# Optimization experiments

Measured on AMD Instinct MI355X. Metric: run time of the kernel, lower is better.

The kernel has to match this reference:

```python
import jax, jax.numpy as jnp
import numpy as np

N_T, N_I = 4096, 4096
TEXT_DIM, IMAGE_DIM, HIDDEN_DIM = 1024, 1024, 1024


def setup_inputs() -> dict:
    key = jax.random.key(0)
    ks = jax.random.split(key, 8)
    s_t = 1.0 / np.sqrt(TEXT_DIM)
    s_i = 1.0 / np.sqrt(IMAGE_DIM)
    return {
        "text_features": jax.random.normal(ks[0], (N_T, TEXT_DIM), jnp.float32),
        "image_features": jax.random.normal(ks[1], (N_I, IMAGE_DIM), jnp.float32),
        # nn.Linear params: weight [out, in], bias [out]
        "w_text": jax.random.uniform(ks[2], (HIDDEN_DIM, TEXT_DIM), jnp.float32, -s_t, s_t),
        "b_text": jax.random.uniform(ks[3], (HIDDEN_DIM,), jnp.float32, -s_t, s_t),
        "w_image": jax.random.uniform(ks[4], (HIDDEN_DIM, IMAGE_DIM), jnp.float32, -s_i, s_i),
        "b_image": jax.random.uniform(ks[5], (HIDDEN_DIM,), jnp.float32, -s_i, s_i),
        "scale_TI": jnp.ones((1,), jnp.float32),
        "scale_IT": jnp.ones((1,), jnp.float32),
    }


def reference(text_features, image_features, w_text, b_text, w_image, b_image, scale_TI, scale_IT):
    # linear projections to shared hidden space
    t = text_features @ w_text.T + b_text      # [N_t, H]
    i = image_features @ w_image.T + b_image   # [N_i, H]
    inv_sqrt_h = 1.0 / jnp.sqrt(jnp.asarray(HIDDEN_DIM, t.dtype))
    # text -> image attention: softmax over image axis, scaled post-softmax
    logits_TI = (t @ i.T) * inv_sqrt_h               # [N_t, N_i]
    attn_TI = jax.nn.softmax(logits_TI, axis=-1) * scale_TI
    # image -> text attention
    attn_IT = jax.nn.softmax(logits_TI.T, axis=-1) * scale_IT  # [N_i, N_t]
    text_attention_on_image = attn_TI @ image_features  # [N_t, image_dim]
    image_attention_on_text = attn_IT @ text_features   # [N_i, text_dim]
    return (text_attention_on_image, image_attention_on_text)
```

## Files before the change

### kernel.cpp

```cpp
#include <hip/hip_runtime.h>


typedef __bf16 bf16x8 __attribute__((ext_vector_type(8)));
typedef float f32x4 __attribute__((ext_vector_type(4)));

#define N_T 4096
#define N_I 4096
#define DIM 1024
#define TSS 136

__device__ __forceinline__ unsigned short f2bf(float f) {
    unsigned int u = __float_as_uint(f);
    u += 0x7fffu + ((u >> 16) & 1u);
    return (unsigned short)(u >> 16);
}

__device__ __forceinline__ void async_cp16(const unsigned short* g, unsigned short* l) {
    __builtin_amdgcn_global_load_lds(
        (const __attribute__((address_space(1))) unsigned int*)g,
        (__attribute__((address_space(3))) unsigned int*)l, 16, 0, 0);
}

__device__ __forceinline__ void stage_async(const unsigned short* __restrict__ src,
                                            int ld, int row0, int k0,
                                            unsigned short* lds, int tid) {
    int r = tid >> 2, c = (tid & 3) << 3;
    const unsigned short* g = src + (size_t)(row0 + r) * ld + k0 + c;
    async_cp16(g, lds + r * 32 + c);
    async_cp16(g + (size_t)64 * ld, lds + (64 + r) * 32 + c);
}

__device__ __forceinline__ void mfma_step(const unsigned short* As,
                                          const unsigned short* Bs, f32x4 acc[4][4],
                                          int wrow, int wcol, int lane16, int quad) {
    bf16x8 a[4], b[4];
#pragma unroll
    for (int i = 0; i < 4; ++i) {
        a[i] = *(const bf16x8*)&As[(wrow + i * 16 + lane16) * 32 + quad * 8];
        b[i] = *(const bf16x8*)&Bs[(wcol + i * 16 + lane16) * 32 + quad * 8];
    }
#pragma unroll
    for (int i = 0; i < 4; ++i)
#pragma unroll
        for (int j = 0; j < 4; ++j)
            acc[i][j] = __builtin_amdgcn_mfma_f32_16x16x32_bf16(a[i], b[j], acc[i][j], 0, 0, 0);
}

__device__ __forceinline__ void tile_store(const unsigned short* sm,
                                           unsigned short* __restrict__ g, int ld,
                                           int row0, int col0, int tid) {
    int r = tid >> 1, h = (tid & 1) << 6;
    const unsigned short* src = sm + r * TSS + h;
    unsigned short* dst = g + (size_t)(row0 + r) * ld + col0 + h;
#pragma unroll
    for (int v = 0; v < 8; ++v)
        *(uint4*)(dst + v * 8) = *(const uint4*)(src + v * 8);
}

#define GEMM_IDX()                                               \
    int tid = threadIdx.x;                                       \
    int m0 = blockIdx.x * 128, n0 = blockIdx.y * 128;            \
    int lane = tid & 63, wave = tid >> 6;                        \
    int lane16 = lane & 15, quad = lane >> 4;                    \
    int wrow = (wave >> 1) * 64, wcol = (wave & 1) * 64;         \
    f32x4 acc[4][4];                                             \
    {                                                            \
        f32x4 z = {0.f, 0.f, 0.f, 0.f};                          \
        for (int i = 0; i < 4; ++i)                              \
            for (int j = 0; j < 4; ++j) acc[i][j] = z;           \
    }

__global__ void __launch_bounds__(256)
cvt_bf16_all(const float* __restrict__ t, const float* __restrict__ im,
             const float* __restrict__ wt, const float* __restrict__ wi,
             unsigned short* __restrict__ tb, unsigned short* __restrict__ imb,
             unsigned short* __restrict__ wtb, unsigned short* __restrict__ wib) {
    size_t i = (size_t)(blockIdx.x * 256 + threadIdx.x) * 8;
    const float* s;
    unsigned short* d;
    size_t off;
    if (i < 4194304)       { s = t;  d = tb;  off = i; }
    else if (i < 8388608)  { s = im; d = imb; off = i - 4194304; }
    else if (i < 9437184)  { s = wt; d = wtb; off = i - 8388608; }
    else                   { s = wi; d = wib; off = i - 9437184; }
    float4 f0 = *(const float4*)(s + off);
    float4 f1 = *(const float4*)(s + off + 4);
    uint4 o;
    o.x = (unsigned int)f2bf(f0.x) | ((unsigned int)f2bf(f0.y) << 16);
    o.y = (unsigned int)f2bf(f0.z) | ((unsigned int)f2bf(f0.w) << 16);
    o.z = (unsigned int)f2bf(f1.x) | ((unsigned int)f2bf(f1.y) << 16);
    o.w = (unsigned int)f2bf(f1.z) | ((unsigned int)f2bf(f1.w) << 16);
    *(uint4*)(d + off) = o;
}

__global__ void __launch_bounds__(256)
transpose_cvt2(const float* __restrict__ im, const float* __restrict__ tx,
               unsigned short* __restrict__ imgT, unsigned short* __restrict__ textT) {
    const float* in = blockIdx.z ? tx : im;
    unsigned short* out = blockIdx.z ? textT : imgT;
    __shared__ float tile[32][33];
    int c0 = blockIdx.x * 32, r0 = blockIdx.y * 32;
    int txi = threadIdx.x & 31, tyi = threadIdx.x >> 5;
#pragma unroll
    for (int i = tyi; i < 32; i += 8)
        tile[i][txi] = in[(size_t)(r0 + i) * DIM + c0 + txi];
    __syncthreads();
#pragma unroll
    for (int i = tyi; i < 32; i += 8)
        out[(size_t)(c0 + i) * N_T + r0 + txi] = f2bf(tile[txi][i]);
}

__global__ void __launch_bounds__(256, 2)
gemm_proj2(const unsigned short* __restrict__ Atx, const unsigned short* __restrict__ Wtx,
           const float* __restrict__ btx, unsigned short* __restrict__ Ctx,
           const unsigned short* __restrict__ Aim, const unsigned short* __restrict__ Wim,
           const float* __restrict__ bim, unsigned short* __restrict__ Cim) {
    __shared__ unsigned short As[128 * 32];
    __shared__ unsigned short Bs[128 * 32];
    int z = blockIdx.z;
    const unsigned short* A = z ? Aim : Atx;
    const unsigned short* W = z ? Wim : Wtx;
    const float* bias = z ? bim : btx;
    unsigned short* C = z ? Cim : Ctx;
    GEMM_IDX();
    for (int k0 = 0; k0 < DIM; k0 += 32) {
        stage_async(A, DIM, m0, k0, As, tid);
        stage_async(W, DIM, n0, k0, Bs, tid);
        __syncthreads();
        mfma_step(As, Bs, acc, wrow, wcol, lane16, quad);
        __syncthreads();
    }
#pragma unroll
    for (int j = 0; j < 4; ++j) {
        int col = n0 + wcol + j * 16 + lane16;
        float bv = bias[col];
#pragma unroll
        for (int i = 0; i < 4; ++i) {
            int rowb = m0 + wrow + i * 16 + quad * 4;
#pragma unroll
            for (int r = 0; r < 4; ++r)
                C[(size_t)(rowb + r) * DIM + col] = f2bf(acc[i][j][r] + bv);
        }
    }
}

__global__ void __launch_bounds__(256, 2)
gemm_logits_exp(const unsigned short* __restrict__ Tb,
                const unsigned short* __restrict__ Ib,
                unsigned short* __restrict__ P, unsigned short* __restrict__ PT,
                float* __restrict__ lT, float* __restrict__ lI) {
    __shared__ unsigned short smem[128 * TSS];
    unsigned short* As = smem;
    unsigned short* Bs = smem + 128 * 32;
    GEMM_IDX();
    for (int k0 = 0; k0 < DIM; k0 += 32) {
        stage_async(Tb, DIM, m0, k0, As, tid);
        stage_async(Ib, DIM, n0, k0, Bs, tid);
        __syncthreads();
        mfma_step(As, Bs, acc, wrow, wcol, lane16, quad);
        __syncthreads();
    }
#pragma unroll
    for (int i = 0; i < 4; ++i)
#pragma unroll
        for (int j = 0; j < 4; ++j)
#pragma unroll
            for (int r = 0; r < 4; ++r)
                acc[i][j][r] = __expf(acc[i][j][r] * 0.03125f);
#pragma unroll
    for (int i = 0; i < 4; ++i)
#pragma unroll
        for (int r = 0; r < 4; ++r) {
            float s = acc[i][0][r] + acc[i][1][r] + acc[i][2][r] + acc[i][3][r];
            s += __shfl_xor(s, 1); s += __shfl_xor(s, 2);
            s += __shfl_xor(s, 4); s += __shfl_xor(s, 8);
            if (lane16 == 0) atomicAdd(&lT[m0 + wrow + i * 16 + quad * 4 + r], s);
        }
#pragma unroll
    for (int j = 0; j < 4; ++j) {
        float s = 0.f;
#pragma unroll
        for (int i = 0; i < 4; ++i)
#pragma unroll
            for (int r = 0; r < 4; ++r) s += acc[i][j][r];
        s += __shfl_xor(s, 16); s += __shfl_xor(s, 32);
        if (quad == 0) atomicAdd(&lI[n0 + wcol + j * 16 + lane16], s);
    }
    __syncthreads();
#pragma unroll
    for (int i = 0; i < 4; ++i)
#pragma unroll
        for (int j = 0; j < 4; ++j)
#pragma unroll
            for (int r = 0; r < 4; ++r)
                smem[(wrow + i * 16 + quad * 4 + r) * TSS + wcol + j * 16 + lane16] =
                    f2bf(acc[i][j][r]);
    __syncthreads();
    tile_store(smem, P, N_I, m0, n0, tid);
    __syncthreads();
#pragma unroll
    for (int i = 0; i < 4; ++i)
#pragma unroll
        for (int j = 0; j < 4; ++j) {
            unsigned int lo = (unsigned int)f2bf(acc[i][j][0]) |
                              ((unsigned int)f2bf(acc[i][j][1]) << 16);
            unsigned int hi = (unsigned int)f2bf(acc[i][j][2]) |
                              ((unsigned int)f2bf(acc[i][j][3]) << 16);
            uint2 v; v.x = lo; v.y = hi;
            *(uint2*)&smem[(wcol + j * 16 + lane16) * TSS + wrow + i * 16 + quad * 4] = v;
        }
    __syncthreads();
    tile_store(smem, PT, N_T, n0, m0, tid);
}

__global__ void __launch_bounds__(256, 2)
gemm_attn2(const unsigned short* __restrict__ P, const unsigned short* __restrict__ imgT,
           const float* __restrict__ lT, const float* __restrict__ sTI,
           float* __restrict__ out0,
           const unsigned short* __restrict__ PT, const unsigned short* __restrict__ textT,
           const float* __restrict__ lI, const float* __restrict__ sIT,
           float* __restrict__ out1) {
    __shared__ unsigned short As[128 * 32];
    __shared__ unsigned short Bs[128 * 32];
    int which = blockIdx.z;
    const unsigned short* A = which ? PT : P;
    const unsigned short* Bt = which ? textT : imgT;
    const float* l = which ? lI : lT;
    const float* sp = which ? sIT : sTI;
    float* out = which ? out1 : out0;
    GEMM_IDX();
    for (int k0 = 0; k0 < 4096; k0 += 32) {
        stage_async(A, 4096, m0, k0, As, tid);
        stage_async(Bt, 4096, n0, k0, Bs, tid);
        __syncthreads();
        mfma_step(As, Bs, acc, wrow, wcol, lane16, quad);
        __syncthreads();
    }
    float sc = sp[0];
#pragma unroll
    for (int i = 0; i < 4; ++i) {
        int rowb = m0 + wrow + i * 16 + quad * 4;
        float fac[4];
#pragma unroll
        for (int r = 0; r < 4; ++r) fac[r] = sc / l[rowb + r];
#pragma unroll
        for (int j = 0; j < 4; ++j) {
            int col = n0 + wcol + j * 16 + lane16;
#pragma unroll
            for (int r = 0; r < 4; ++r)
                out[(size_t)(rowb + r) * DIM + col] = acc[i][j][r] * fac[r];
        }
    }
}

extern "C" void kernel_launch(void* const* d_in, const int* in_sizes, int n_in,
                              void* d_out, int out_size, void* d_ws, size_t ws_size,
                              hipStream_t stream) {
    const float* text = (const float*)d_in[0];
    const float* image = (const float*)d_in[1];
    const float* w_text = (const float*)d_in[2];
    const float* b_text = (const float*)d_in[3];
    const float* w_image = (const float*)d_in[4];
    const float* b_image = (const float*)d_in[5];
    const float* scale_TI = (const float*)d_in[6];
    const float* scale_IT = (const float*)d_in[7];
    float* out0 = (float*)d_out;
    float* out1 = out0 + (size_t)N_T * DIM;

    char* ws = (char*)d_ws;
    unsigned short* text_bf = (unsigned short*)(ws);
    unsigned short* image_bf = (unsigned short*)(ws + (8ull << 20));
    unsigned short* wt_bf = (unsigned short*)(ws + (16ull << 20));
    unsigned short* wi_bf = (unsigned short*)(ws + (18ull << 20));
    unsigned short* P = (unsigned short*)(ws);
    unsigned short* imgT = (unsigned short*)(ws + (32ull << 20));
    unsigned short* textT = (unsigned short*)(ws + (40ull << 20));
    unsigned short* t_bf = (unsigned short*)(ws + (48ull << 20));
    unsigned short* i_bf = (unsigned short*)(ws + (56ull << 20));
    unsigned short* PT = (unsigned short*)(ws + (64ull << 20));
    float* lT = (float*)(ws + (96ull << 20));
    float* lI = (float*)(ws + (96ull << 20) + 16384);

    hipMemsetAsync(lT, 0, 32768, stream);

    cvt_bf16_all<<<5120, 256, 0, stream>>>(text, image, w_text, w_image,
                                           text_bf, image_bf, wt_bf, wi_bf);
    transpose_cvt2<<<dim3(DIM / 32, N_T / 32, 2), 256, 0, stream>>>(image, text, imgT, textT);

    gemm_proj2<<<dim3(N_T / 128, DIM / 128, 2), 256, 0, stream>>>(
        text_bf, wt_bf, b_text, t_bf, image_bf, wi_bf, b_image, i_bf);

    gemm_logits_exp<<<dim3(N_T / 128, N_I / 128), 256, 0, stream>>>(t_bf, i_bf, P, PT, lT, lI);

    gemm_attn2<<<dim3(N_T / 128, DIM / 128, 2), 256, 0, stream>>>(
        P, imgT, lT, scale_TI, out0, PT, textT, lI, scale_IT, out1);
}
```

Baseline: 290.6 us.

## Split K across two thread halves in attention GEMM with LDS reduction

The attention-output GEMM now launches 512 threads per block, and each 256-thread half computes half of the 4096-long K range into its own LDS buffers. The two partial accumulators are then summed through LDS before the normalising epilogue. The goal is more waves in flight per output tile to hide memory latency in this long-K GEMM. In exchange it adds reduction traffic and extra barriers, and the launch bounds of (512,4) may squeeze registers and cause spills.

```diff
diff --git a/kernel.cpp b/kernel.cpp
--- a/kernel.cpp
+++ b/kernel.cpp
@@ -23,8 +23,8 @@
 
 __device__ __forceinline__ void stage_async(const unsigned short* __restrict__ src,
                                             int ld, int row0, int k0,
-                                            unsigned short* lds, int tid) {
-    int r = tid >> 2, c = (tid & 3) << 3;
+                                            unsigned short* lds, int t) {
+    int r = t >> 2, c = (t & 3) << 3;
     const unsigned short* g = src + (size_t)(row0 + r) * ld + k0 + c;
     async_cp16(g, lds + r * 32 + c);
     async_cp16(g + (size_t)64 * ld, lds + (64 + r) * 32 + c);
@@ -213,29 +213,64 @@
     tile_store(smem, PT, N_T, n0, m0, tid);
 }
 
-__global__ void __launch_bounds__(256, 2)
+__global__ void __launch_bounds__(512, 4)
 gemm_attn2(const unsigned short* __restrict__ P, const unsigned short* __restrict__ imgT,
            const float* __restrict__ lT, const float* __restrict__ sTI,
            float* __restrict__ out0,
            const unsigned short* __restrict__ PT, const unsigned short* __restrict__ textT,
            const float* __restrict__ lI, const float* __restrict__ sIT,
            float* __restrict__ out1) {
-    __shared__ unsigned short As[128 * 32];
-    __shared__ unsigned short Bs[128 * 32];
+    __shared__ unsigned short As[2][128 * 32];
+    __shared__ unsigned short Bs[2][128 * 32];
     int which = blockIdx.z;
     const unsigned short* A = which ? PT : P;
     const unsigned short* Bt = which ? textT : imgT;
     const float* l = which ? lI : lT;
     const float* sp = which ? sIT : sTI;
     float* out = which ? out1 : out0;
-    GEMM_IDX();
-    for (int k0 = 0; k0 < 4096; k0 += 32) {
-        stage_async(A, 4096, m0, k0, As, tid);
-        stage_async(Bt, 4096, n0, k0, Bs, tid);
-        __syncthreads();
-        mfma_step(As, Bs, acc, wrow, wcol, lane16, quad);
-        __syncthreads();
-    }
+
+    int tid = threadIdx.x;
+    int half = tid >> 8;
+    int t = tid & 255;
+    int m0 = blockIdx.x * 128, n0 = blockIdx.y * 128;
+    int lane = tid & 63;
+    int wv = (tid >> 6) & 3;
+    int lane16 = lane & 15, quad = lane >> 4;
+    int wrow = (wv >> 1) * 64, wcol = (wv & 1) * 64;
+    f32x4 acc[4][4];
+    {
+        f32x4 z = {0.f, 0.f, 0.f, 0.f};
+        for (int i = 0; i < 4; ++i)
+            for (int j = 0; j < 4; ++j) acc[i][j] = z;
+    }
+
+    int kbeg = half * 2048, kend = kbeg + 2048;
+    for (int k0 = kbeg; k0 < kend; k0 += 32) {
+        stage_async(A, 4096, m0, k0, As[half], t);
+        stage_async(Bt, 4096, n0, k0, Bs[half], t);
+        __syncthreads();
+        mfma_step(As[half], Bs[half], acc, wrow, wcol, lane16, quad);
+        __syncthreads();
+    }
+
+    float* red = (float*)As;
+#pragma unroll
+    for (int i = 0; i < 4; ++i) {
+        __syncthreads();
+        if (half) {
+#pragma unroll
+            for (int j = 0; j < 4; ++j)
+                *(f32x4*)&red[wv * 1024 + lane * 16 + j * 4] = acc[i][j];
+        }
+        __syncthreads();
+        if (!half) {
+#pragma unroll
+            for (int j = 0; j < 4; ++j)
+                acc[i][j] += *(const f32x4*)&red[wv * 1024 + lane * 16 + j * 4];
+        }
+    }
+    if (half) return;
+
     float sc = sp[0];
 #pragma unroll
     for (int i = 0; i < 4; ++i) {
@@ -292,6 +327,6 @@
 
     gemm_logits_exp<<<dim3(N_T / 128, N_I / 128), 256, 0, stream>>>(t_bf, i_bf, P, PT, lT, lI);
 
-    gemm_attn2<<<dim3(N_T / 128, DIM / 128, 2), 256, 0, stream>>>(
+    gemm_attn2<<<dim3(N_T / 128, DIM / 128, 2), 512, 0, stream>>>(
         P, imgT, lT, scale_TI, out0, PT, textT, lI, scale_IT, out1);
 }
```

Measured after the change: 279.9 us. 3.7% less time.
